# Performance work log

Measured on AMD Instinct MI355X. Metric: run time of the kernel, lower is better.

Reference implementation:

```python
import jax, jax.numpy as jnp
import numpy as np

B, C, H, W = 16, 3, 384, 1280
EPS = 1e-7


def setup_inputs() -> dict:
    key = jax.random.key(0)
    k1, k2, k3, k4 = jax.random.split(key, 4)
    source_image = jax.random.normal(k1, (B, C, H, W), jnp.float32)
    depth_map = jax.random.uniform(k2, (B, 1, H, W), jnp.float32, minval=0.1, maxval=80.0)
    pose = 0.05 * jax.random.normal(k3, (B, 6), jnp.float32)
    # realistic KITTI-style pinhole intrinsics, per-batch mild perturbation
    base = jnp.array([[0.58 * W, 0.0, 0.5 * W],
                      [0.0, 1.92 * H, 0.5 * H],
                      [0.0, 0.0, 1.0]], jnp.float32)
    noise = 1.0 + 0.01 * jax.random.normal(k4, (B, 3, 3), jnp.float32)
    intrinsic = base[None] * noise  # zero entries stay zero -> invertible
    return {"source_image": source_image, "depth_map": depth_map,
            "pose": pose, "intrinsic": intrinsic}


def rot_from_axisangle(aa):
    # aa: [B,3] -> [B,3,3] (Rodrigues)
    theta = jnp.linalg.norm(aa, axis=-1, keepdims=True)  # [B,1]
    axis = aa / (theta + EPS)
    c = jnp.cos(theta)
    s = jnp.sin(theta)
    t = 1.0 - c
    x, y, z = axis[:, 0:1], axis[:, 1:2], axis[:, 2:3]
    row0 = jnp.concatenate([t * x * x + c, t * x * y - s * z, t * z * x + s * y], axis=1)
    row1 = jnp.concatenate([t * x * y + s * z, t * y * y + c, t * y * z - s * x], axis=1)
    row2 = jnp.concatenate([t * z * x - s * y, t * y * z + s * x, t * z * z + c], axis=1)
    return jnp.stack([row0, row1, row2], axis=1)  # [B,3,3]


def bilinear_grid_sample(img, gx, gy):
    # img: [B,C,H,W]; gx,gy: [B,H,W] in [-1,1]; align_corners=True, padding zeros
    Bc, Cc, Hc, Wc = img.shape
    x = (gx + 1.0) * 0.5 * (Wc - 1)
    y = (gy + 1.0) * 0.5 * (Hc - 1)
    x0 = jnp.floor(x)
    y0 = jnp.floor(y)
    x1 = x0 + 1.0
    y1 = y0 + 1.0
    wx1 = x - x0
    wx0 = 1.0 - wx1
    wy1 = y - y0
    wy0 = 1.0 - wy1
    imgf = img.reshape(Bc, Cc, Hc * Wc)

    def gather(xi, yi):
        inb = ((xi >= 0) & (xi <= Wc - 1) & (yi >= 0) & (yi <= Hc - 1)).astype(img.dtype)
        xc = jnp.clip(xi, 0, Wc - 1).astype(jnp.int32)
        yc = jnp.clip(yi, 0, Hc - 1).astype(jnp.int32)
        idx = (yc * Wc + xc).reshape(Bc, 1, -1)
        vals = jnp.take_along_axis(imgf, jnp.broadcast_to(idx, (Bc, Cc, idx.shape[-1])), axis=2)
        return vals.reshape(Bc, Cc, Hc, Wc) * inb[:, None]

    out = (gather(x0, y0) * (wx0 * wy0)[:, None]
           + gather(x1, y0) * (wx1 * wy0)[:, None]
           + gather(x0, y1) * (wx0 * wy1)[:, None]
           + gather(x1, y1) * (wx1 * wy1)[:, None])
    return out


def reference(source_image, depth_map, pose, intrinsic):
    Bb, _, Hh, Ww = depth_map.shape
    # pixel grid, homogeneous [H,W,3] = (x, y, 1)
    ys, xs = jnp.meshgrid(jnp.arange(Hh, dtype=depth_map.dtype),
                          jnp.arange(Ww, dtype=depth_map.dtype), indexing='ij')
    pix = jnp.stack([xs, ys, jnp.ones_like(xs)], axis=-1)  # [H,W,3]
    # backproject: K^{-1} @ pix * depth
    inv_K = jnp.linalg.inv(intrinsic)  # [B,3,3]
    cam = jnp.einsum('bij,hwj->bhwi', inv_K, pix)  # [B,H,W,3]
    frustum = cam * jnp.transpose(depth_map, (0, 2, 3, 1))  # [B,H,W,3]
    # rigid transform
    R = rot_from_axisangle(pose[:, :3])  # [B,3,3]
    t = pose[:, 3:]  # [B,3]
    points = jnp.einsum('bij,bhwj->bhwi', R, frustum) + t[:, None, None, :]
    # project with K
    coord = jnp.einsum('bij,bhwj->bhwi', intrinsic, points)  # [B,H,W,3]
    z = coord[..., 2] + EPS
    px = coord[..., 0] / z
    py = coord[..., 1] / z
    gx = px / (Ww - 1) * 2.0 - 1.0
    gy = py / (Hh - 1) * 2.0 - 1.0
    return bilinear_grid_sample(source_image, gx, gy)
```

## Files before the change

kernel.cpp:

```cpp
#include <hip/hip_runtime.h>

#define B_ 16
#define C_ 3
#define H_ 384
#define W_ 1280
#define HW_ (H_*W_)
#define EPS_ 1e-7f

typedef float v2f __attribute__((ext_vector_type(2)));

__device__ __forceinline__ v2f load2(const float* p) {
  v2f r;
  __builtin_memcpy(&r, p, 8);
  return r;
}

__device__ __forceinline__ void mat3mul(const float* A, const float* Bm, float* C) {
  #pragma unroll
  for (int i = 0; i < 3; i++)
    #pragma unroll
    for (int j = 0; j < 3; j++)
      C[i*3+j] = A[i*3+0]*Bm[0*3+j] + A[i*3+1]*Bm[1*3+j] + A[i*3+2]*Bm[2*3+j];
}

__device__ void compute_MT(const float* __restrict__ pose,
                           const float* __restrict__ intr,
                           int b, float* M, float* T)
{
  float K[9];
  #pragma unroll
  for (int i = 0; i < 9; i++) K[i] = intr[b*9 + i];
  float aa0 = pose[b*6 + 0], aa1 = pose[b*6 + 1], aa2 = pose[b*6 + 2];
  float t0  = pose[b*6 + 3], t1  = pose[b*6 + 4], t2  = pose[b*6 + 5];

  float theta = sqrtf(aa0*aa0 + aa1*aa1 + aa2*aa2);
  float invn  = 1.0f / (theta + EPS_);
  float x = aa0*invn, y = aa1*invn, z = aa2*invn;
  float c = cosf(theta), s = sinf(theta), t = 1.0f - c;
  float R[9] = {
    t*x*x + c,   t*x*y - s*z, t*z*x + s*y,
    t*x*y + s*z, t*y*y + c,   t*y*z - s*x,
    t*z*x - s*y, t*y*z + s*x, t*z*z + c
  };

  float a = K[0], bb = K[1], cc = K[2];
  float d = K[3], e  = K[4], f  = K[5];
  float g = K[6], h  = K[7], ii = K[8];
  float A0 = e*ii - f*h, A1 = f*g - d*ii, A2 = d*h - e*g;
  float id = 1.0f / (a*A0 + bb*A1 + cc*A2);
  float iK[9] = {
    A0*id, (cc*h - bb*ii)*id, (bb*f - cc*e)*id,
    A1*id, (a*ii - cc*g)*id,  (cc*d - a*f)*id,
    A2*id, (bb*g - a*h)*id,   (a*e  - bb*d)*id
  };

  float KR[9];
  mat3mul(K, R, KR);
  mat3mul(KR, iK, M);
  T[0] = K[0]*t0 + K[1]*t1 + K[2]*t2;
  T[1] = K[3]*t0 + K[4]*t1 + K[5]*t2;
  T[2] = K[6]*t0 + K[7]*t1 + K[8]*t2;
}

__global__ __launch_bounds__(256) void warp_kernel(
    const float* __restrict__ src,
    const float* __restrict__ depth,
    const float* __restrict__ pose,
    const float* __restrict__ intr,
    float* __restrict__ out)
{
  __shared__ float sp[12];
  int b = blockIdx.y;
  if (threadIdx.x == 0) {
    float M[9], T[3];
    compute_MT(pose, intr, b, M, T);
    #pragma unroll
    for (int i = 0; i < 9; i++) sp[i] = M[i];
    #pragma unroll
    for (int i = 0; i < 3; i++) sp[9 + i] = T[i];
  }
  __syncthreads();
  float m00 = sp[0], m01 = sp[1], m02 = sp[2];
  float m10 = sp[3], m11 = sp[4], m12 = sp[5];
  float m20 = sp[6], m21 = sp[7], m22 = sp[8];
  float T0  = sp[9], T1  = sp[10], T2 = sp[11];

  int p = blockIdx.x * 256 + threadIdx.x;
  int j = p % W_;
  int i = p / W_;

  float d  = depth[(size_t)b * HW_ + p];
  float xf = (float)j, yf = (float)i;

  float cx = (m00*xf + m01*yf + m02)*d + T0;
  float cy = (m10*xf + m11*yf + m12)*d + T1;
  float cz = (m20*xf + m21*yf + m22)*d + T2;
  float inv = 1.0f / (cz + EPS_);
  float px = cx * inv;
  float py = cy * inv;

  float x0f = floorf(px), y0f = floorf(py);
  float x1f = x0f + 1.0f, y1f = y0f + 1.0f;
  float wx1 = px - x0f, wx0 = 1.0f - wx1;
  float wy1 = py - y0f, wy0 = 1.0f - wy1;

  float mx0 = (x0f >= 0.0f && x0f <= (float)(W_-1)) ? 1.0f : 0.0f;
  float mx1 = (x1f >= 0.0f && x1f <= (float)(W_-1)) ? 1.0f : 0.0f;
  float my0 = (y0f >= 0.0f && y0f <= (float)(H_-1)) ? 1.0f : 0.0f;
  float my1 = (y1f >= 0.0f && y1f <= (float)(H_-1)) ? 1.0f : 0.0f;

  int xc0 = (int)fminf(fmaxf(x0f, 0.0f), (float)(W_-1));
  int xc1 = (int)fminf(fmaxf(x1f, 0.0f), (float)(W_-1));
  int yc0 = (int)fminf(fmaxf(y0f, 0.0f), (float)(H_-1));
  int yc1 = (int)fminf(fmaxf(y1f, 0.0f), (float)(H_-1));

  float w00 = wx0*wy0*mx0*my0;
  float w01 = wx1*wy0*mx1*my0;
  float w10 = wx0*wy1*mx0*my1;
  float w11 = wx1*wy1*mx1*my1;

  int base = xc0 < (W_-2) ? xc0 : (W_-2);
  bool s0 = (xc0 == base);
  bool s1 = (xc1 == base + 1);
  float wax = (s0 ? w00 : 0.0f) + (s1 ? 0.0f : w01);
  float way = (s0 ? 0.0f : w00) + (s1 ? w01 : 0.0f);
  float wbx = (s0 ? w10 : 0.0f) + (s1 ? 0.0f : w11);
  float wby = (s0 ? 0.0f : w10) + (s1 ? w11 : 0.0f);

  int rb0 = yc0*W_ + base;
  int rb1 = yc1*W_ + base;

  size_t sb = (size_t)b * C_ * HW_;
  size_t op = (size_t)p;
  const float* s0p = src + sb;
  const float* s1p = s0p + HW_;
  const float* s2p = s1p + HW_;

  v2f a0 = load2(s0p + rb0);
  v2f b0 = load2(s0p + rb1);
  v2f a1 = load2(s1p + rb0);
  v2f b1 = load2(s1p + rb1);
  v2f a2 = load2(s2p + rb0);
  v2f b2 = load2(s2p + rb1);

  float v0 = a0.x*wax + a0.y*way + b0.x*wbx + b0.y*wby;
  float v1 = a1.x*wax + a1.y*way + b1.x*wbx + b1.y*wby;
  float v2 = a2.x*wax + a2.y*way + b2.x*wbx + b2.y*wby;

  __builtin_nontemporal_store(v0, &out[sb + op]);
  __builtin_nontemporal_store(v1, &out[sb + HW_ + op]);
  __builtin_nontemporal_store(v2, &out[sb + 2*(size_t)HW_ + op]);
}

extern "C" void kernel_launch(void* const* d_in, const int* in_sizes, int n_in,
                              void* d_out, int out_size, void* d_ws, size_t ws_size,
                              hipStream_t stream) {
  const float* src   = (const float*)d_in[0];
  const float* depth = (const float*)d_in[1];
  const float* pose  = (const float*)d_in[2];
  const float* intr  = (const float*)d_in[3];
  float* out = (float*)d_out;

  dim3 grid(HW_ / 256, B_);
  warp_kernel<<<grid, 256, 0, stream>>>(src, depth, pose, intr, out);
}
```

Measured before the change: 240.9 us.

## Tile blocks as 256-column by 2-row bands with XCD-aware block remapping

```diff
diff --git a/kernel.cpp b/kernel.cpp
--- a/kernel.cpp
+++ b/kernel.cpp
@@ -6,6 +6,13 @@
 #define W_ 1280
 #define HW_ (H_*W_)
 #define EPS_ 1e-7f
+
+#define COLS_ 256
+#define ROWS_ 2
+#define BANDS_ (W_/COLS_)
+#define RTILES_ (H_/ROWS_)
+#define NBLK_ (BANDS_*RTILES_*B_)
+#define NXCD_ 8
 
 typedef float v2f __attribute__((ext_vector_type(2)));
 
@@ -70,7 +77,14 @@
     float* __restrict__ out)
 {
   __shared__ float sp[12];
-  int b = blockIdx.y;
+
+  int l = blockIdx.x;
+  int w = (l & (NXCD_-1)) * (NBLK_/NXCD_) + (l >> 3);
+  int rt   = w % RTILES_;
+  int tmp  = w / RTILES_;
+  int band = tmp % BANDS_;
+  int b    = tmp / BANDS_;
+
   if (threadIdx.x == 0) {
     float M[9], T[3];
     compute_MT(pose, intr, b, M, T);
@@ -85,71 +99,85 @@
   float m20 = sp[6], m21 = sp[7], m22 = sp[8];
   float T0  = sp[9], T1  = sp[10], T2 = sp[11];
 
-  int p = blockIdx.x * 256 + threadIdx.x;
-  int j = p % W_;
-  int i = p / W_;
+  int j  = band * COLS_ + threadIdx.x;
+  int i0 = rt * ROWS_;
+  float xf = (float)j;
 
-  float d  = depth[(size_t)b * HW_ + p];
-  float xf = (float)j, yf = (float)i;
-
-  float cx = (m00*xf + m01*yf + m02)*d + T0;
-  float cy = (m10*xf + m11*yf + m12)*d + T1;
-  float cz = (m20*xf + m21*yf + m22)*d + T2;
-  float inv = 1.0f / (cz + EPS_);
-  float px = cx * inv;
-  float py = cy * inv;
-
-  float x0f = floorf(px), y0f = floorf(py);
-  float x1f = x0f + 1.0f, y1f = y0f + 1.0f;
-  float wx1 = px - x0f, wx0 = 1.0f - wx1;
-  float wy1 = py - y0f, wy0 = 1.0f - wy1;
-
-  float mx0 = (x0f >= 0.0f && x0f <= (float)(W_-1)) ? 1.0f : 0.0f;
-  float mx1 = (x1f >= 0.0f && x1f <= (float)(W_-1)) ? 1.0f : 0.0f;
-  float my0 = (y0f >= 0.0f && y0f <= (float)(H_-1)) ? 1.0f : 0.0f;
-  float my1 = (y1f >= 0.0f && y1f <= (float)(H_-1)) ? 1.0f : 0.0f;
-
-  int xc0 = (int)fminf(fmaxf(x0f, 0.0f), (float)(W_-1));
-  int xc1 = (int)fminf(fmaxf(x1f, 0.0f), (float)(W_-1));
-  int yc0 = (int)fminf(fmaxf(y0f, 0.0f), (float)(H_-1));
-  int yc1 = (int)fminf(fmaxf(y1f, 0.0f), (float)(H_-1));
-
-  float w00 = wx0*wy0*mx0*my0;
-  float w01 = wx1*wy0*mx1*my0;
-  float w10 = wx0*wy1*mx0*my1;
-  float w11 = wx1*wy1*mx1*my1;
-
-  int base = xc0 < (W_-2) ? xc0 : (W_-2);
-  bool s0 = (xc0 == base);
-  bool s1 = (xc1 == base + 1);
-  float wax = (s0 ? w00 : 0.0f) + (s1 ? 0.0f : w01);
-  float way = (s0 ? 0.0f : w00) + (s1 ? w01 : 0.0f);
-  float wbx = (s0 ? w10 : 0.0f) + (s1 ? 0.0f : w11);
-  float wby = (s0 ? 0.0f : w10) + (s1 ? w11 : 0.0f);
-
-  int rb0 = yc0*W_ + base;
-  int rb1 = yc1*W_ + base;
+  float ax = m00*xf + m02;
+  float ay = m10*xf + m12;
+  float az = m20*xf + m22;
 
   size_t sb = (size_t)b * C_ * HW_;
-  size_t op = (size_t)p;
   const float* s0p = src + sb;
   const float* s1p = s0p + HW_;
   const float* s2p = s1p + HW_;
 
-  v2f a0 = load2(s0p + rb0);
-  v2f b0 = load2(s0p + rb1);
-  v2f a1 = load2(s1p + rb0);
-  v2f b1 = load2(s1p + rb1);
-  v2f a2 = load2(s2p + rb0);
-  v2f b2 = load2(s2p + rb1);
+  const float* dp = depth + (size_t)b * HW_ + (size_t)i0 * W_ + j;
+  float dv[ROWS_];
+  #pragma unroll
+  for (int r = 0; r < ROWS_; r++)
+    dv[r] = __builtin_nontemporal_load(dp + r * W_);
 
-  float v0 = a0.x*wax + a0.y*way + b0.x*wbx + b0.y*wby;
-  float v1 = a1.x*wax + a1.y*way + b1.x*wbx + b1.y*wby;
-  float v2 = a2.x*wax + a2.y*way + b2.x*wbx + b2.y*wby;
+  #pragma unroll
+  for (int r = 0; r < ROWS_; r++) {
+    int i = i0 + r;
+    float yf = (float)i;
+    float d  = dv[r];
 
-  __builtin_nontemporal_store(v0, &out[sb + op]);
-  __builtin_nontemporal_store(v1, &out[sb + HW_ + op]);
-  __builtin_nontemporal_store(v2, &out[sb + 2*(size_t)HW_ + op]);
+    float cx = (ax + m01*yf)*d + T0;
+    float cy = (ay + m11*yf)*d + T1;
+    float cz = (az + m21*yf)*d + T2;
+    float inv = 1.0f / (cz + EPS_);
+    float px = cx * inv;
+    float py = cy * inv;
+
+    float x0f = floorf(px), y0f = floorf(py);
+    float x1f = x0f + 1.0f, y1f = y0f + 1.0f;
+    float wx1 = px - x0f, wx0 = 1.0f - wx1;
+    float wy1 = py - y0f, wy0 = 1.0f - wy1;
+
+    float mx0 = (x0f >= 0.0f && x0f <= (float)(W_-1)) ? 1.0f : 0.0f;
+    float mx1 = (x1f >= 0.0f && x1f <= (float)(W_-1)) ? 1.0f : 0.0f;
+    float my0 = (y0f >= 0.0f && y0f <= (float)(H_-1)) ? 1.0f : 0.0f;
+    float my1 = (y1f >= 0.0f && y1f <= (float)(H_-1)) ? 1.0f : 0.0f;
+
+    int xc0 = (int)fminf(fmaxf(x0f, 0.0f), (float)(W_-1));
+    int xc1 = (int)fminf(fmaxf(x1f, 0.0f), (float)(W_-1));
+    int yc0 = (int)fminf(fmaxf(y0f, 0.0f), (float)(H_-1));
+    int yc1 = (int)fminf(fmaxf(y1f, 0.0f), (float)(H_-1));
+
+    float w00 = wx0*wy0*mx0*my0;
+    float w01 = wx1*wy0*mx1*my0;
+    float w10 = wx0*wy1*mx0*my1;
+    float w11 = wx1*wy1*mx1*my1;
+
+    int base = xc0 < (W_-2) ? xc0 : (W_-2);
+    bool sl0 = (xc0 == base);
+    bool sl1 = (xc1 == base + 1);
+    float wax = (sl0 ? w00 : 0.0f) + (sl1 ? 0.0f : w01);
+    float way = (sl0 ? 0.0f : w00) + (sl1 ? w01 : 0.0f);
+    float wbx = (sl0 ? w10 : 0.0f) + (sl1 ? 0.0f : w11);
+    float wby = (sl0 ? 0.0f : w10) + (sl1 ? w11 : 0.0f);
+
+    int rb0 = yc0*W_ + base;
+    int rb1 = yc1*W_ + base;
+
+    v2f a0 = load2(s0p + rb0);
+    v2f b0 = load2(s0p + rb1);
+    v2f a1 = load2(s1p + rb0);
+    v2f b1 = load2(s1p + rb1);
+    v2f a2 = load2(s2p + rb0);
+    v2f b2 = load2(s2p + rb1);
+
+    float v0 = a0.x*wax + a0.y*way + b0.x*wbx + b0.y*wby;
+    float v1 = a1.x*wax + a1.y*way + b1.x*wbx + b1.y*wby;
+    float v2 = a2.x*wax + a2.y*way + b2.x*wbx + b2.y*wby;
+
+    size_t op = (size_t)i * W_ + j;
+    __builtin_nontemporal_store(v0, &out[sb + op]);
+    __builtin_nontemporal_store(v1, &out[sb + HW_ + op]);
+    __builtin_nontemporal_store(v2, &out[sb + 2*(size_t)HW_ + op]);
+  }
 }
 
 extern "C" void kernel_launch(void* const* d_in, const int* in_sizes, int n_in,
@@ -161,6 +189,6 @@
   const float* intr  = (const float*)d_in[3];
   float* out = (float*)d_out;
 
-  dim3 grid(HW_ / 256, B_);
+  dim3 grid(NBLK_);
   warp_kernel<<<grid, 256, 0, stream>>>(src, depth, pose, intr, out);
 }
```

New measurement: 251.8 us. 4.5% more time.

## Repack source to interleaved fp16 and swizzle blocks across XCDs

Applied to the files above, without the earlier changes.

```diff
diff --git a/kernel.cpp b/kernel.cpp
--- a/kernel.cpp
+++ b/kernel.cpp
@@ -1,4 +1,5 @@
 #include <hip/hip_runtime.h>
+#include <hip/hip_fp16.h>
 
 #define B_ 16
 #define C_ 3
@@ -7,12 +8,17 @@
 #define HW_ (H_*W_)
 #define EPS_ 1e-7f
 
+#define NXCD_ 8
+#define NBLK2_ (B_*H_*(W_/256))
+#define CPX2_  (NBLK2_/NXCD_)
+
 typedef float v2f __attribute__((ext_vector_type(2)));
 
 __device__ __forceinline__ v2f load2(const float* p) {
-  v2f r;
-  __builtin_memcpy(&r, p, 8);
-  return r;
+  v2f r; __builtin_memcpy(&r, p, 8); return r;
+}
+__device__ __forceinline__ uint4 load16u(const void* p) {
+  uint4 r; __builtin_memcpy(&r, p, 16); return r;
 }
 
 __device__ __forceinline__ void mat3mul(const float* A, const float* Bm, float* C) {
@@ -62,22 +68,54 @@
   T[2] = K[6]*t0 + K[7]*t1 + K[8]*t2;
 }
 
-__global__ __launch_bounds__(256) void warp_kernel(
-    const float* __restrict__ src,
+__global__ __launch_bounds__(256) void repack_kernel(
+    const float* __restrict__ src, uint4* __restrict__ ws)
+{
+  int tg = blockIdx.x * 256 + threadIdx.x;
+  int b  = tg / (HW_/2);
+  int p  = (tg - b * (HW_/2)) * 2;
+  const float* s = src + (size_t)b * 3 * HW_ + p;
+  v2f c0 = load2(s);
+  v2f c1 = load2(s + HW_);
+  v2f c2 = load2(s + 2*HW_);
+  __half2 h0 = __floats2half2_rn(c0.x, c1.x);
+  __half2 h1 = __floats2half2_rn(c2.x, 0.0f);
+  __half2 h2 = __floats2half2_rn(c0.y, c1.y);
+  __half2 h3 = __floats2half2_rn(c2.y, 0.0f);
+  uint4 o;
+  o.x = *(unsigned*)&h0; o.y = *(unsigned*)&h1;
+  o.z = *(unsigned*)&h2; o.w = *(unsigned*)&h3;
+  ws[tg] = o;
+}
+
+__global__ __launch_bounds__(256) void warp2_kernel(
+    const uint4* __restrict__ pk,
     const float* __restrict__ depth,
     const float* __restrict__ pose,
     const float* __restrict__ intr,
     float* __restrict__ out)
 {
   __shared__ float sp[12];
-  int b = blockIdx.y;
+
+  int l = blockIdx.x;
+  int w = (l & (NXCD_-1)) * CPX2_ + (l >> 3);
+  int r    = w % H_;
+  int tmp  = w / H_;
+  int band = tmp % (W_/256);
+  int b    = tmp / (W_/256);
+
+  int j = band * 256 + threadIdx.x;
+  int i = r;
+
+  float d = depth[(size_t)b * HW_ + (size_t)i * W_ + j];
+
   if (threadIdx.x == 0) {
     float M[9], T[3];
     compute_MT(pose, intr, b, M, T);
     #pragma unroll
-    for (int i = 0; i < 9; i++) sp[i] = M[i];
-    #pragma unroll
-    for (int i = 0; i < 3; i++) sp[9 + i] = T[i];
+    for (int k = 0; k < 9; k++) sp[k] = M[k];
+    #pragma unroll
+    for (int k = 0; k < 3; k++) sp[9 + k] = T[k];
   }
   __syncthreads();
   float m00 = sp[0], m01 = sp[1], m02 = sp[2];
@@ -85,13 +123,7 @@
   float m20 = sp[6], m21 = sp[7], m22 = sp[8];
   float T0  = sp[9], T1  = sp[10], T2 = sp[11];
 
-  int p = blockIdx.x * 256 + threadIdx.x;
-  int j = p % W_;
-  int i = p / W_;
-
-  float d  = depth[(size_t)b * HW_ + p];
   float xf = (float)j, yf = (float)i;
-
   float cx = (m00*xf + m01*yf + m02)*d + T0;
   float cy = (m10*xf + m11*yf + m12)*d + T1;
   float cz = (m20*xf + m21*yf + m22)*d + T2;
@@ -127,26 +159,109 @@
   float wbx = (s0 ? w10 : 0.0f) + (s1 ? 0.0f : w11);
   float wby = (s0 ? 0.0f : w10) + (s1 ? w11 : 0.0f);
 
+  const char* pkb = (const char*)pk;
+  size_t offA = ((size_t)b * HW_ + (size_t)yc0 * W_ + base) * 8;
+  size_t offB = ((size_t)b * HW_ + (size_t)yc1 * W_ + base) * 8;
+
+  uint4 RA = load16u(pkb + offA);
+  uint4 RB = load16u(pkb + offB);
+  __builtin_amdgcn_sched_barrier(0);
+
+  float2 A0 = __half22float2(*(const __half2*)&RA.x);
+  float  A2 = __low2float  (*(const __half2*)&RA.y);
+  float2 A1 = __half22float2(*(const __half2*)&RA.z);
+  float  A3 = __low2float  (*(const __half2*)&RA.w);
+  float2 B0 = __half22float2(*(const __half2*)&RB.x);
+  float  B2 = __low2float  (*(const __half2*)&RB.y);
+  float2 B1 = __half22float2(*(const __half2*)&RB.z);
+  float  B3 = __low2float  (*(const __half2*)&RB.w);
+
+  float v0 = A0.x*wax + A1.x*way + B0.x*wbx + B1.x*wby;
+  float v1 = A0.y*wax + A1.y*way + B0.y*wbx + B1.y*wby;
+  float v2 = A2  *wax + A3  *way + B2  *wbx + B3  *wby;
+
+  size_t sb = (size_t)b * C_ * HW_;
+  size_t op = (size_t)i * W_ + j;
+  __builtin_nontemporal_store(v0, &out[sb + op]);
+  __builtin_nontemporal_store(v1, &out[sb + HW_ + op]);
+  __builtin_nontemporal_store(v2, &out[sb + 2*(size_t)HW_ + op]);
+}
+
+__global__ __launch_bounds__(256) void warp_fb_kernel(
+    const float* __restrict__ src,
+    const float* __restrict__ depth,
+    const float* __restrict__ pose,
+    const float* __restrict__ intr,
+    float* __restrict__ out)
+{
+  __shared__ float sp[12];
+  int b = blockIdx.y;
+  if (threadIdx.x == 0) {
+    float M[9], T[3];
+    compute_MT(pose, intr, b, M, T);
+    #pragma unroll
+    for (int k = 0; k < 9; k++) sp[k] = M[k];
+    #pragma unroll
+    for (int k = 0; k < 3; k++) sp[9 + k] = T[k];
+  }
+  __syncthreads();
+  float m00 = sp[0], m01 = sp[1], m02 = sp[2];
+  float m10 = sp[3], m11 = sp[4], m12 = sp[5];
+  float m20 = sp[6], m21 = sp[7], m22 = sp[8];
+  float T0  = sp[9], T1  = sp[10], T2 = sp[11];
+
+  int p = blockIdx.x * 256 + threadIdx.x;
+  int j = p % W_;
+  int i = p / W_;
+
+  float d  = depth[(size_t)b * HW_ + p];
+  float xf = (float)j, yf = (float)i;
+  float cx = (m00*xf + m01*yf + m02)*d + T0;
+  float cy = (m10*xf + m11*yf + m12)*d + T1;
+  float cz = (m20*xf + m21*yf + m22)*d + T2;
+  float inv = 1.0f / (cz + EPS_);
+  float px = cx * inv, py = cy * inv;
+
+  float x0f = floorf(px), y0f = floorf(py);
+  float x1f = x0f + 1.0f, y1f = y0f + 1.0f;
+  float wx1 = px - x0f, wx0 = 1.0f - wx1;
+  float wy1 = py - y0f, wy0 = 1.0f - wy1;
+  float mx0 = (x0f >= 0.0f && x0f <= (float)(W_-1)) ? 1.0f : 0.0f;
+  float mx1 = (x1f >= 0.0f && x1f <= (float)(W_-1)) ? 1.0f : 0.0f;
+  float my0 = (y0f >= 0.0f && y0f <= (float)(H_-1)) ? 1.0f : 0.0f;
+  float my1 = (y1f >= 0.0f && y1f <= (float)(H_-1)) ? 1.0f : 0.0f;
+  int xc0 = (int)fminf(fmaxf(x0f, 0.0f), (float)(W_-1));
+  int xc1 = (int)fminf(fmaxf(x1f, 0.0f), (float)(W_-1));
+  int yc0 = (int)fminf(fmaxf(y0f, 0.0f), (float)(H_-1));
+  int yc1 = (int)fminf(fmaxf(y1f, 0.0f), (float)(H_-1));
+  float w00 = wx0*wy0*mx0*my0;
+  float w01 = wx1*wy0*mx1*my0;
+  float w10 = wx0*wy1*mx0*my1;
+  float w11 = wx1*wy1*mx1*my1;
+  int base = xc0 < (W_-2) ? xc0 : (W_-2);
+  bool s0 = (xc0 == base);
+  bool s1 = (xc1 == base + 1);
+  float wax = (s0 ? w00 : 0.0f) + (s1 ? 0.0f : w01);
+  float way = (s0 ? 0.0f : w00) + (s1 ? w01 : 0.0f);
+  float wbx = (s0 ? w10 : 0.0f) + (s1 ? 0.0f : w11);
+  float wby = (s0 ? 0.0f : w10) + (s1 ? w11 : 0.0f);
   int rb0 = yc0*W_ + base;
   int rb1 = yc1*W_ + base;
 
   size_t sb = (size_t)b * C_ * HW_;
-  size_t op = (size_t)p;
   const float* s0p = src + sb;
   const float* s1p = s0p + HW_;
   const float* s2p = s1p + HW_;
-
   v2f a0 = load2(s0p + rb0);
   v2f b0 = load2(s0p + rb1);
   v2f a1 = load2(s1p + rb0);
   v2f b1 = load2(s1p + rb1);
   v2f a2 = load2(s2p + rb0);
   v2f b2 = load2(s2p + rb1);
-
   float v0 = a0.x*wax + a0.y*way + b0.x*wbx + b0.y*wby;
   float v1 = a1.x*wax + a1.y*way + b1.x*wbx + b1.y*wby;
   float v2 = a2.x*wax + a2.y*way + b2.x*wbx + b2.y*wby;
-
+  size_t op = (size_t)p;
   __builtin_nontemporal_store(v0, &out[sb + op]);
   __builtin_nontemporal_store(v1, &out[sb + HW_ + op]);
   __builtin_nontemporal_store(v2, &out[sb + 2*(size_t)HW_ + op]);
@@ -161,6 +276,13 @@
   const float* intr  = (const float*)d_in[3];
   float* out = (float*)d_out;
 
-  dim3 grid(HW_ / 256, B_);
-  warp_kernel<<<grid, 256, 0, stream>>>(src, depth, pose, intr, out);
-}
+  const size_t need = (size_t)B_ * HW_ * 8;
+  if (d_ws != nullptr && ws_size >= need) {
+    uint4* ws = (uint4*)d_ws;
+    repack_kernel<<<dim3(B_*HW_/2/256), 256, 0, stream>>>(src, ws);
+    warp2_kernel<<<dim3(NBLK2_), 256, 0, stream>>>(ws, depth, pose, intr, out);
+  } else {
+    dim3 grid(HW_ / 256, B_);
+    warp_fb_kernel<<<grid, 256, 0, stream>>>(src, depth, pose, intr, out);
+  }
+}
```

Result: faster. 234.8 us (-2.5%).

## Repack source image to interleaved fp16 and gather with 2-pixel tiled warp kernel

Applied to the files above, without the earlier changes.

```diff
diff --git a/kernel.cpp b/kernel.cpp
--- a/kernel.cpp
+++ b/kernel.cpp
@@ -1,4 +1,5 @@
 #include <hip/hip_runtime.h>
+#include <hip/hip_fp16.h>
 
 #define B_ 16
 #define C_ 3
@@ -7,12 +8,32 @@
 #define HW_ (H_*W_)
 #define EPS_ 1e-7f
 
+#define NXCD_ 8
+
+#define BANDS_ (W_/256)
+#define RTILES_ (H_/2)
+#define NBLK3_ (BANDS_*RTILES_*B_)
+#define CPX3_  (NBLK3_/NXCD_)
+
 typedef float v2f __attribute__((ext_vector_type(2)));
+typedef float v4f __attribute__((ext_vector_type(4)));
 
 __device__ __forceinline__ v2f load2(const float* p) {
-  v2f r;
-  __builtin_memcpy(&r, p, 8);
-  return r;
+  v2f r; __builtin_memcpy(&r, p, 8); return r;
+}
+__device__ __forceinline__ uint4 load16u(const void* p) {
+  uint4 r; __builtin_memcpy(&r, p, 16); return r;
+}
+__device__ __forceinline__ v4f ntload4(const float* p) {
+  return __builtin_nontemporal_load((const v4f*)p);
+}
+__device__ __forceinline__ void storent2(float* p, float a, float b) {
+  v2f r; r.x = a; r.y = b;
+  __builtin_nontemporal_store(r, (v2f*)p);
+}
+__device__ __forceinline__ unsigned pack2(float a, float b) {
+  __half2 h = __floats2half2_rn(a, b);
+  unsigned u; __builtin_memcpy(&u, &h, 4); return u;
 }
 
 __device__ __forceinline__ void mat3mul(const float* A, const float* Bm, float* C) {
@@ -62,7 +83,163 @@
   T[2] = K[6]*t0 + K[7]*t1 + K[8]*t2;
 }
 
-__global__ __launch_bounds__(256) void warp_kernel(
+__global__ __launch_bounds__(256) void repack_kernel(
+    const float* __restrict__ src, uint4* __restrict__ ws)
+{
+  int tg = blockIdx.x * 256 + threadIdx.x;
+  int b  = tg / (HW_/4);
+  int p  = (tg - b * (HW_/4)) * 4;
+  const float* s = src + (size_t)b * 3 * HW_ + p;
+  v4f c0 = ntload4(s);
+  v4f c1 = ntload4(s + HW_);
+  v4f c2 = ntload4(s + 2*HW_);
+  uint4 o0, o1;
+  o0.x = pack2(c0.x, c1.x); o0.y = pack2(c2.x, 0.0f);
+  o0.z = pack2(c0.y, c1.y); o0.w = pack2(c2.y, 0.0f);
+  o1.x = pack2(c0.z, c1.z); o1.y = pack2(c2.z, 0.0f);
+  o1.z = pack2(c0.w, c1.w); o1.w = pack2(c2.w, 0.0f);
+  ws[(size_t)tg*2]     = o0;
+  ws[(size_t)tg*2 + 1] = o1;
+}
+
+__global__ __launch_bounds__(256) void warp2_kernel(
+    const uint4* __restrict__ pk,
+    const float* __restrict__ depth,
+    const float* __restrict__ pose,
+    const float* __restrict__ intr,
+    float* __restrict__ out)
+{
+  __shared__ float sp[12];
+
+  int l = blockIdx.x;
+  int w = (l & (NXCD_-1)) * CPX3_ + (l >> 3);
+  int rt   = w % RTILES_;
+  int tmp  = w / RTILES_;
+  int band = tmp % BANDS_;
+  int b    = tmp / BANDS_;
+
+  int t  = threadIdx.x;
+  int rr = t >> 7;
+  int cp = t & 127;
+  int j0 = band * 256 + 2*cp;
+  int i  = rt * 2 + rr;
+
+  v2f dq = load2(depth + (size_t)b * HW_ + (size_t)i * W_ + j0);
+
+  if (t == 0) {
+    float M[9], T[3];
+    compute_MT(pose, intr, b, M, T);
+    #pragma unroll
+    for (int k = 0; k < 9; k++) sp[k] = M[k];
+    #pragma unroll
+    for (int k = 0; k < 3; k++) sp[9 + k] = T[k];
+  }
+  __syncthreads();
+  float m00 = sp[0], m01 = sp[1], m02 = sp[2];
+  float m10 = sp[3], m11 = sp[4], m12 = sp[5];
+  float m20 = sp[6], m21 = sp[7], m22 = sp[8];
+  float T0  = sp[9], T1  = sp[10], T2 = sp[11];
+
+  float yf = (float)i;
+  float bx = m01*yf + m02;
+  float by = m11*yf + m12;
+  float bz = m21*yf + m22;
+
+  const char* pkb = (const char*)pk;
+  size_t pb = (size_t)b * HW_;
+
+  float xfA = (float)j0;
+  float dA  = dq.x;
+  float czA = (m20*xfA + bz)*dA + T2;
+  float ivA = 1.0f / (czA + EPS_);
+  float pxA = ((m00*xfA + bx)*dA + T0) * ivA;
+  float pyA = ((m10*xfA + by)*dA + T1) * ivA;
+  float x0A = floorf(pxA), y0A = floorf(pyA);
+  float fx1A = pxA - x0A, fx0A = 1.0f - fx1A;
+  float fy1A = pyA - y0A, fy0A = 1.0f - fy1A;
+  float wx0A = fx0A * ((x0A >= 0.0f && x0A <= (float)(W_-1)) ? 1.0f : 0.0f);
+  float wx1A = fx1A * ((x0A+1.0f >= 0.0f && x0A+1.0f <= (float)(W_-1)) ? 1.0f : 0.0f);
+  float wy0A = fy0A * ((y0A >= 0.0f && y0A <= (float)(H_-1)) ? 1.0f : 0.0f);
+  float wy1A = fy1A * ((y0A+1.0f >= 0.0f && y0A+1.0f <= (float)(H_-1)) ? 1.0f : 0.0f);
+  int xc0A = (int)fminf(fmaxf(x0A, 0.0f), (float)(W_-1));
+  int xc1A = (int)fminf(fmaxf(x0A+1.0f, 0.0f), (float)(W_-1));
+  int yc0A = (int)fminf(fmaxf(y0A, 0.0f), (float)(H_-1));
+  int yc1A = (int)fminf(fmaxf(y0A+1.0f, 0.0f), (float)(H_-1));
+  float w00A = wx0A*wy0A, w01A = wx1A*wy0A, w10A = wx0A*wy1A, w11A = wx1A*wy1A;
+  int baseA = xc0A < (W_-2) ? xc0A : (W_-2);
+  bool s0A = (xc0A == baseA), s1A = (xc1A == baseA + 1);
+  float waxA = (s0A ? w00A : 0.0f) + (s1A ? 0.0f : w01A);
+  float wayA = (s0A ? 0.0f : w00A) + (s1A ? w01A : 0.0f);
+  float wbxA = (s0A ? w10A : 0.0f) + (s1A ? 0.0f : w11A);
+  float wbyA = (s0A ? 0.0f : w10A) + (s1A ? w11A : 0.0f);
+  size_t offA0 = (pb + (size_t)yc0A * W_ + baseA) * 8;
+  size_t offA1 = (pb + (size_t)yc1A * W_ + baseA) * 8;
+
+  float xfB = (float)(j0 + 1);
+  float dB  = dq.y;
+  float czB = (m20*xfB + bz)*dB + T2;
+  float ivB = 1.0f / (czB + EPS_);
+  float pxB = ((m00*xfB + bx)*dB + T0) * ivB;
+  float pyB = ((m10*xfB + by)*dB + T1) * ivB;
+  float x0B = floorf(pxB), y0B = floorf(pyB);
+  float fx1B = pxB - x0B, fx0B = 1.0f - fx1B;
+  float fy1B = pyB - y0B, fy0B = 1.0f - fy1B;
+  float wx0B = fx0B * ((x0B >= 0.0f && x0B <= (float)(W_-1)) ? 1.0f : 0.0f);
+  float wx1B = fx1B * ((x0B+1.0f >= 0.0f && x0B+1.0f <= (float)(W_-1)) ? 1.0f : 0.0f);
+  float wy0B = fy0B * ((y0B >= 0.0f && y0B <= (float)(H_-1)) ? 1.0f : 0.0f);
+  float wy1B = fy1B * ((y0B+1.0f >= 0.0f && y0B+1.0f <= (float)(H_-1)) ? 1.0f : 0.0f);
+  int xc0B = (int)fminf(fmaxf(x0B, 0.0f), (float)(W_-1));
+  int xc1B = (int)fminf(fmaxf(x0B+1.0f, 0.0f), (float)(W_-1));
+  int yc0B = (int)fminf(fmaxf(y0B, 0.0f), (float)(H_-1));
+  int yc1B = (int)fminf(fmaxf(y0B+1.0f, 0.0f), (float)(H_-1));
+  float w00B = wx0B*wy0B, w01B = wx1B*wy0B, w10B = wx0B*wy1B, w11B = wx1B*wy1B;
+  int baseB = xc0B < (W_-2) ? xc0B : (W_-2);
+  bool s0B = (xc0B == baseB), s1B = (xc1B == baseB + 1);
+  float waxB = (s0B ? w00B : 0.0f) + (s1B ? 0.0f : w01B);
+  float wayB = (s0B ? 0.0f : w00B) + (s1B ? w01B : 0.0f);
+  float wbxB = (s0B ? w10B : 0.0f) + (s1B ? 0.0f : w11B);
+  float wbyB = (s0B ? 0.0f : w10B) + (s1B ? w11B : 0.0f);
+  size_t offB0 = (pb + (size_t)yc0B * W_ + baseB) * 8;
+  size_t offB1 = (pb + (size_t)yc1B * W_ + baseB) * 8;
+
+  uint4 RA0 = load16u(pkb + offA0);
+  uint4 RA1 = load16u(pkb + offA1);
+  uint4 RB0 = load16u(pkb + offB0);
+  uint4 RB1 = load16u(pkb + offB1);
+  __builtin_amdgcn_sched_barrier(0);
+
+  float2 A00 = __half22float2(*(const __half2*)&RA0.x);
+  float  A02 = __low2float  (*(const __half2*)&RA0.y);
+  float2 A01 = __half22float2(*(const __half2*)&RA0.z);
+  float  A03 = __low2float  (*(const __half2*)&RA0.w);
+  float2 A10 = __half22float2(*(const __half2*)&RA1.x);
+  float  A12 = __low2float  (*(const __half2*)&RA1.y);
+  float2 A11 = __half22float2(*(const __half2*)&RA1.z);
+  float  A13 = __low2float  (*(const __half2*)&RA1.w);
+  float vA0 = A00.x*waxA + A01.x*wayA + A10.x*wbxA + A11.x*wbyA;
+  float vA1 = A00.y*waxA + A01.y*wayA + A10.y*wbxA + A11.y*wbyA;
+  float vA2 = A02  *waxA + A03  *wayA + A12  *wbxA + A13  *wbyA;
+
+  float2 B00 = __half22float2(*(const __half2*)&RB0.x);
+  float  B02 = __low2float  (*(const __half2*)&RB0.y);
+  float2 B01 = __half22float2(*(const __half2*)&RB0.z);
+  float  B03 = __low2float  (*(const __half2*)&RB0.w);
+  float2 B10 = __half22float2(*(const __half2*)&RB1.x);
+  float  B12 = __low2float  (*(const __half2*)&RB1.y);
+  float2 B11 = __half22float2(*(const __half2*)&RB1.z);
+  float  B13 = __low2float  (*(const __half2*)&RB1.w);
+  float vB0 = B00.x*waxB + B01.x*wayB + B10.x*wbxB + B11.x*wbyB;
+  float vB1 = B00.y*waxB + B01.y*wayB + B10.y*wbxB + B11.y*wbyB;
+  float vB2 = B02  *waxB + B03  *wayB + B12  *wbxB + B13  *wbyB;
+
+  size_t sb = (size_t)b * C_ * HW_;
+  size_t op = (size_t)i * W_ + j0;
+  storent2(out + sb + op,                   vA0, vB0);
+  storent2(out + sb + HW_ + op,             vA1, vB1);
+  storent2(out + sb + 2*(size_t)HW_ + op,   vA2, vB2);
+}
+
+__global__ __launch_bounds__(256) void warp_fb_kernel(
     const float* __restrict__ src,
     const float* __restrict__ depth,
     const float* __restrict__ pose,
@@ -75,9 +252,9 @@
     float M[9], T[3];
     compute_MT(pose, intr, b, M, T);
     #pragma unroll
-    for (int i = 0; i < 9; i++) sp[i] = M[i];
-    #pragma unroll
-    for (int i = 0; i < 3; i++) sp[9 + i] = T[i];
+    for (int k = 0; k < 9; k++) sp[k] = M[k];
+    #pragma unroll
+    for (int k = 0; k < 3; k++) sp[9 + k] = T[k];
   }
   __syncthreads();
   float m00 = sp[0], m01 = sp[1], m02 = sp[2];
@@ -91,34 +268,28 @@
 
   float d  = depth[(size_t)b * HW_ + p];
   float xf = (float)j, yf = (float)i;
-
   float cx = (m00*xf + m01*yf + m02)*d + T0;
   float cy = (m10*xf + m11*yf + m12)*d + T1;
   float cz = (m20*xf + m21*yf + m22)*d + T2;
   float inv = 1.0f / (cz + EPS_);
-  float px = cx * inv;
-  float py = cy * inv;
+  float px = cx * inv, py = cy * inv;
 
   float x0f = floorf(px), y0f = floorf(py);
   float x1f = x0f + 1.0f, y1f = y0f + 1.0f;
   float wx1 = px - x0f, wx0 = 1.0f - wx1;
   float wy1 = py - y0f, wy0 = 1.0f - wy1;
-
   float mx0 = (x0f >= 0.0f && x0f <= (float)(W_-1)) ? 1.0f : 0.0f;
   float mx1 = (x1f >= 0.0f && x1f <= (float)(W_-1)) ? 1.0f : 0.0f;
   float my0 = (y0f >= 0.0f && y0f <= (float)(H_-1)) ? 1.0f : 0.0f;
   float my1 = (y1f >= 0.0f && y1f <= (float)(H_-1)) ? 1.0f : 0.0f;
-
   int xc0 = (int)fminf(fmaxf(x0f, 0.0f), (float)(W_-1));
   int xc1 = (int)fminf(fmaxf(x1f, 0.0f), (float)(W_-1));
   int yc0 = (int)fminf(fmaxf(y0f, 0.0f), (float)(H_-1));
   int yc1 = (int)fminf(fmaxf(y1f, 0.0f), (float)(H_-1));
-
   float w00 = wx0*wy0*mx0*my0;
   float w01 = wx1*wy0*mx1*my0;
   float w10 = wx0*wy1*mx0*my1;
   float w11 = wx1*wy1*mx1*my1;
-
   int base = xc0 < (W_-2) ? xc0 : (W_-2);
   bool s0 = (xc0 == base);
   bool s1 = (xc1 == base + 1);
@@ -126,27 +297,23 @@
   float way = (s0 ? 0.0f : w00) + (s1 ? w01 : 0.0f);
   float wbx = (s0 ? w10 : 0.0f) + (s1 ? 0.0f : w11);
   float wby = (s0 ? 0.0f : w10) + (s1 ? w11 : 0.0f);
-
   int rb0 = yc0*W_ + base;
   int rb1 = yc1*W_ + base;
 
   size_t sb = (size_t)b * C_ * HW_;
-  size_t op = (size_t)p;
   const float* s0p = src + sb;
   const float* s1p = s0p + HW_;
   const float* s2p = s1p + HW_;
-
   v2f a0 = load2(s0p + rb0);
   v2f b0 = load2(s0p + rb1);
   v2f a1 = load2(s1p + rb0);
   v2f b1 = load2(s1p + rb1);
   v2f a2 = load2(s2p + rb0);
   v2f b2 = load2(s2p + rb1);
-
   float v0 = a0.x*wax + a0.y*way + b0.x*wbx + b0.y*wby;
   float v1 = a1.x*wax + a1.y*way + b1.x*wbx + b1.y*wby;
   float v2 = a2.x*wax + a2.y*way + b2.x*wbx + b2.y*wby;
-
+  size_t op = (size_t)p;
   __builtin_nontemporal_store(v0, &out[sb + op]);
   __builtin_nontemporal_store(v1, &out[sb + HW_ + op]);
   __builtin_nontemporal_store(v2, &out[sb + 2*(size_t)HW_ + op]);
@@ -161,6 +328,13 @@
   const float* intr  = (const float*)d_in[3];
   float* out = (float*)d_out;
 
-  dim3 grid(HW_ / 256, B_);
-  warp_kernel<<<grid, 256, 0, stream>>>(src, depth, pose, intr, out);
-}
+  const size_t need = (size_t)B_ * HW_ * 8;
+  if (d_ws != nullptr && ws_size >= need) {
+    uint4* ws = (uint4*)d_ws;
+    repack_kernel<<<dim3(B_*HW_/4/256), 256, 0, stream>>>(src, ws);
+    warp2_kernel<<<dim3(NBLK3_), 256, 0, stream>>>(ws, depth, pose, intr, out);
+  } else {
+    dim3 grid(HW_ / 256, B_);
+    warp_fb_kernel<<<grid, 256, 0, stream>>>(src, depth, pose, intr, out);
+  }
+}
```

Measured after the change: 231.2 us. 4.0% less time.
